# Performance work log

Measured on AMD Instinct MI355X. Metric: run time of the kernel, lower is better.

The kernel has to match this reference:

```python
import jax, jax.numpy as jnp
import numpy as np

NUM_SPHERICAL = 7
NUM_RADIAL = 6
CUTOFF = 5.0
ENVELOPE_EXPONENT = 5
ENVELOPE_CUTOFF = 5.0  # hardcoded in the torch module: poly_envelop(cutoff=5.0, ...)
E = 1_000_000   # num edges
T = 4_000_000   # num triplets (angles)


def _jn_np(l, x):
    """Spherical Bessel j_l(x) in numpy via upward recurrence (x > 0)."""
    j0 = np.sin(x) / x
    if l == 0:
        return j0
    j1 = np.sin(x) / x ** 2 - np.cos(x) / x
    for i in range(2, l + 1):
        j0, j1 = j1, (2 * i - 1) / x * j1 - j0
    return j1


def _jn_zeros(n, k):
    """First k positive zeros of j_l for l=0..n-1 (zeros interlace)."""
    zeros = np.zeros((n, k))
    prev = np.arange(1, k + n) * np.pi  # zeros of j_0
    zeros[0] = prev[:k]
    for l in range(1, n):
        cur = []
        for i in range(len(prev) - 1):
            a, b = prev[i], prev[i + 1]
            fa = _jn_np(l, a)
            for _ in range(80):  # bisection
                m = 0.5 * (a + b)
                fm = _jn_np(l, m)
                if np.sign(fm) == np.sign(fa):
                    a, fa = m, fm
                else:
                    b = m
            cur.append(0.5 * (a + b))
        prev = np.array(cur)
        zeros[l] = prev[:k]
    return zeros


# constants derived from (num_spherical, num_radial) at build time
Z = _jn_zeros(NUM_SPHERICAL, NUM_RADIAL)  # [S, R] Bessel zeros z_{l,n}
NORM = np.array([[np.sqrt(2.0) / abs(_jn_np(l + 1, Z[l, n])) for n in range(NUM_RADIAL)]
                 for l in range(NUM_SPHERICAL)])  # [S, R]
Y_NORM = np.array([np.sqrt((2 * l + 1) / (4.0 * np.pi)) for l in range(NUM_SPHERICAL)])  # m=0 SH norms


def _spherical_jn(l, a):
    """j_l(a) in jax via upward recurrence."""
    j0 = jnp.sin(a) / a
    if l == 0:
        return j0
    j1 = jnp.sin(a) / a ** 2 - jnp.cos(a) / a
    for i in range(2, l + 1):
        j0, j1 = j1, (2 * i - 1) / a * j1 - j0
    return j1


def _envelope(d):
    """DimeNet polynomial envelope, p = exponent + 1, on u = d / cutoff."""
    p = ENVELOPE_EXPONENT + 1
    a = -(p + 1) * (p + 2) / 2.0
    b = float(p * (p + 2))
    c = -p * (p + 1) / 2.0
    u = d / ENVELOPE_CUTOFF
    env = 1.0 / u + a * u ** (p - 1) + b * u ** p + c * u ** (p + 1)
    return jnp.where(u < 1.0, env, 0.0)


def setup_inputs() -> dict:
    key = jax.random.key(0)
    k1, k2, k3 = jax.random.split(key, 3)
    d = jax.random.uniform(k1, (E,), jnp.float32, 0.5, CUTOFF)           # edge distances
    Angles = jax.random.uniform(k2, (T,), jnp.float32, 0.0, float(np.pi))  # triplet angles
    edge_index_1 = jax.random.randint(k3, (T,), 0, E, dtype=jnp.int64 if jax.config.jax_enable_x64 else jnp.int32)
    return {"d": d, "Angles": Angles, "edge_index_1": edge_index_1}


def reference(d, Angles, edge_index_1):
    S, R = NUM_SPHERICAL, NUM_RADIAL
    zeros = jnp.asarray(Z, d.dtype)     # [S, R]
    norm = jnp.asarray(NORM, d.dtype)   # [S, R]
    x = d / CUTOFF                      # [E]
    # radial basis: norm_{l,n} * j_l(z_{l,n} * x)  -> [E, S, R]
    rbf = jnp.stack([norm[l] * _spherical_jn(l, zeros[l][None, :] * x[:, None])
                     for l in range(S)], axis=1)
    rbf_env = (_envelope(d)[:, None, None] * rbf).reshape(d.shape[0], S * R)  # [E, S*R]
    rbf_env = rbf_env[edge_index_1]  # gather triplets -> [T, S*R]
    # angular basis: Y_l^0(theta) = sqrt((2l+1)/4pi) * P_l(cos theta)
    c = jnp.cos(Angles)
    P = [jnp.ones_like(c), c]
    for l in range(2, S):
        P.append(((2 * l - 1) * c * P[l - 1] - (l - 1) * P[l - 2]) / l)
    y_norm = jnp.asarray(Y_NORM, c.dtype)
    cbf = jnp.stack([y_norm[l] * P[l] for l in range(S)], axis=1)  # [T, S]
    cbf = jnp.repeat(cbf, R, axis=1)  # repeat_interleave -> [T, S*R]
    return rbf_env * cbf
```

## Files before the change

kernel.cpp:

```cpp
#include <hip/hip_runtime.h>
#include <hip/hip_bf16.h>
#include <hip/hip_fp16.h>
#include <math.h>

#define NSPH 7
#define NRAD 6
#define NJ 42
#define ROWH 44
#define BLK 256

typedef float v2 __attribute__((ext_vector_type(2)));

struct KC {
  float zf[NJ];
  float izf[NJ];
  float nyf[NJ];
  float sc5[7];
  float sc6[7];
};

__global__ void __launch_bounds__(BLK, 4) k_fused(const float* __restrict__ d,
                                                  const float* __restrict__ ang,
                                                  const int* __restrict__ idx,
                                                  float* __restrict__ out,
                                                  int T, KC C) {
  __shared__ __half sv[BLK * ROWH];
  const int tid = threadIdx.x;
  const int t0 = blockIdx.x * BLK;
  const int t = t0 + tid;

  if (t < T) {
    const int e = __builtin_nontemporal_load(idx + t);
    const float an = __builtin_nontemporal_load(ang + t);
    const float dv = d[e];

    const float x = dv * 0.2f;
    const float invx = __builtin_amdgcn_rcpf(x);
    const float x2 = x * x;
    const float x5 = x2 * x2 * x;
    float env = invx + x5 * fmaf(x, fmaf(x, -21.0f, 48.0f), -28.0f);
    if (x >= 1.0f) env = 0.0f;

    const float cth = __cosf(an);
    float mP[NSPH];
    {
      float p0 = 1.f, p1 = cth;
      mP[0] = env; mP[1] = env * cth;
      const float rl[5] = {1.f/2.f, 1.f/3.f, 1.f/4.f, 1.f/5.f, 1.f/6.f};
      #pragma unroll
      for (int l = 2; l < NSPH; ++l) {
        float pn = (fmaf((float)(2*l-1) * cth, p1, -(float)(l-1) * p0)) * rl[l-2];
        mP[l] = env * pn;
        p0 = p1; p1 = pn;
      }
    }

    __half* row = sv + tid * ROWH;

    #pragma unroll
    for (int l = 0; l < 5; ++l) {
      #pragma unroll
      for (int p = 0; p < 3; ++p) {
        const int i = l * NRAD + 2 * p;
        v2 z    = {C.zf[i],  C.zf[i+1]};
        v2 iz   = {C.izf[i], C.izf[i+1]};
        v2 ny   = {C.nyf[i], C.nyf[i+1]};
        v2 a    = z * x;
        v2 s;  s.x = __sinf(a.x);  s.y = __sinf(a.y);
        v2 inva = iz * invx;
        v2 j0   = s * inva;
        v2 jl;
        if (l == 0) {
          jl = j0;
        } else {
          v2 c;  c.x = __cosf(a.x);  c.y = __cosf(a.y);
          v2 j1 = (j0 - c) * inva;
          #pragma unroll
          for (int m = 2; m <= l; ++m) {
            v2 jn_ = ((float)(2*m-1) * inva) * j1 - j0;
            j0 = j1; j1 = jn_;
          }
          jl = j1;
        }
        v2 jv = (ny * jl) * mP[l];
        *(__half2*)(row + i) = __float22half2_rn((float2){jv.x, jv.y});
      }
    }

    #pragma unroll
    for (int l = 5; l < NSPH; ++l) {
      const float* sc = (l == 5) ? C.sc5 : C.sc6;
      #pragma unroll
      for (int p = 0; p < 3; ++p) {
        const int i = l * NRAD + 2 * p;
        v2 z    = {C.zf[i],  C.zf[i+1]};
        v2 iz   = {C.izf[i], C.izf[i+1]};
        v2 ny   = {C.nyf[i], C.nyf[i+1]};
        v2 a    = z * x;
        v2 s;  s.x = __sinf(a.x);  s.y = __sinf(a.y);
        v2 c;  c.x = __cosf(a.x);  c.y = __cosf(a.y);
        v2 inva = iz * invx;
        v2 j0   = s * inva;
        v2 j1   = (j0 - c) * inva;
        #pragma unroll
        for (int m = 2; m <= l; ++m) {
          v2 jn_ = ((float)(2*m-1) * inva) * j1 - j0;
          j0 = j1; j1 = jn_;
        }
        v2 u  = a * a;
        v2 pp = u * sc[6] + sc[5];
        pp = u * pp + sc[4];
        pp = u * pp + sc[3];
        pp = u * pp + sc[2];
        pp = u * pp + sc[1];
        pp = u * pp + sc[0];
        v2 u2 = u * u;
        v2 al = (l == 5) ? (u2 * a) : (u2 * u);
        v2 jser = al * pp;
        v2 jl;
        jl.x = (a.x < 4.0f) ? jser.x : j1.x;
        jl.y = (a.y < 4.0f) ? jser.y : j1.y;
        v2 jv = (ny * jl) * mP[l];
        *(__half2*)(row + i) = __float22half2_rn((float2){jv.x, jv.y});
      }
    }
  }
  __syncthreads();

  v2* obase = (v2*)(out + (size_t)t0 * NJ);
  #pragma unroll
  for (int k = 0; k < 21; ++k) {
    unsigned w = k * BLK + tid;
    unsigned tl = w / 21u;
    unsigned jp = w - tl * 21u;
    if ((int)(t0 + tl) < T) {
      __half2 hh = *(const __half2*)(sv + tl * ROWH + 2 * jp);
      float2 r = __half22float2(hh);
      obase[w] = (v2){r.x, r.y};
    }
  }
}

static double jn_host(int l, double x) {
  double j0 = sin(x) / x;
  if (l == 0) return j0;
  double j1 = sin(x) / (x * x) - cos(x) / x;
  for (int i = 2; i <= l; ++i) {
    double jn_ = (2 * i - 1) / x * j1 - j0;
    j0 = j1; j1 = jn_;
  }
  return j1;
}

extern "C" void kernel_launch(void* const* d_in, const int* in_sizes, int n_in,
                              void* d_out, int out_size, void* d_ws, size_t ws_size,
                              hipStream_t stream) {
  const float* d   = (const float*)d_in[0];
  const float* ang = (const float*)d_in[1];
  const int*   idx = (const int*)d_in[2];
  float* out = (float*)d_out;
  const int T = in_sizes[1];

  KC C;
  {
    const double PI = 3.14159265358979323846;
    double zeros[NSPH][NRAD];
    double prev[NSPH + NRAD - 1];
    int np_ = NSPH + NRAD - 1;
    for (int i = 0; i < np_; ++i) prev[i] = (i + 1) * PI;
    for (int j = 0; j < NRAD; ++j) zeros[0][j] = prev[j];
    for (int l = 1; l < NSPH; ++l) {
      int nc = np_ - 1;
      double cur[NSPH + NRAD - 1];
      for (int i = 0; i < nc; ++i) {
        double a = prev[i], b = prev[i + 1];
        double fa = jn_host(l, a);
        for (int it = 0; it < 80; ++it) {
          double m = 0.5 * (a + b);
          double fm = jn_host(l, m);
          if ((fm > 0.0) == (fa > 0.0)) { a = m; fa = fm; } else { b = m; }
        }
        cur[i] = 0.5 * (a + b);
      }
      for (int i = 0; i < nc; ++i) prev[i] = cur[i];
      np_ = nc;
      for (int j = 0; j < NRAD; ++j) zeros[l][j] = prev[j];
    }
    for (int l = 0; l < NSPH; ++l) {
      double yn = sqrt((2.0 * l + 1.0) / (4.0 * PI));
      for (int n = 0; n < NRAD; ++n) {
        int i = l * NRAD + n;
        double z = zeros[l][n];
        C.zf[i]  = (float)z;
        C.izf[i] = (float)(1.0 / z);
        C.nyf[i] = (float)(sqrt(2.0) / fabs(jn_host(l + 1, z)) * yn);
      }
    }
    for (int l = 5; l <= 6; ++l) {
      double dfact = 1.0;
      for (int m = 2 * l + 1; m > 1; m -= 2) dfact *= m;
      double ck = 1.0 / dfact;
      float* sc = (l == 5) ? C.sc5 : C.sc6;
      sc[0] = (float)ck;
      for (int k = 1; k < 7; ++k) {
        ck = -ck / (2.0 * k * (2 * l + 2 * k + 1));
        sc[k] = (float)ck;
      }
    }
  }

  k_fused<<<(T + BLK - 1) / BLK, BLK, 0, stream>>>(d, ang, idx, out, T, C);
}
```

Before: 177.6 us.

## Use per-wave LDS slices, drop block barrier, widen nontemporal output stores

Each wave now writes its 64 triplets into its own unpadded LDS slice and reads them back after only an LDS waitcnt, replacing the block-wide __syncthreads. The transpose-out loop now issues 16-byte nontemporal stores instead of 8-byte stores, and the half conversion uses the packed round-toward-zero instruction. The aim is to remove barrier stalls, cut the number of store instructions and avoid cache pollution. The risks are LDS bank conflicts from removing the row padding and slightly different rounding, since round-toward-zero replaces round-to-nearest.

```diff
diff --git a/kernel.cpp b/kernel.cpp
--- a/kernel.cpp
+++ b/kernel.cpp
@@ -6,10 +6,11 @@
 #define NSPH 7
 #define NRAD 6
 #define NJ 42
-#define ROWH 44
 #define BLK 256
 
 typedef float v2 __attribute__((ext_vector_type(2)));
+typedef float v4 __attribute__((ext_vector_type(4)));
+typedef __fp16 h2 __attribute__((ext_vector_type(2)));
 
 struct KC {
   float zf[NJ];
@@ -24,10 +25,14 @@
                                                   const int* __restrict__ idx,
                                                   float* __restrict__ out,
                                                   int T, KC C) {
-  __shared__ __half sv[BLK * ROWH];
-  const int tid = threadIdx.x;
-  const int t0 = blockIdx.x * BLK;
-  const int t = t0 + tid;
+  __shared__ __half sv[BLK * NJ];
+  const int tid  = threadIdx.x;
+  const int lane = tid & 63;
+  const int wave = tid >> 6;
+  const int tw = blockIdx.x * BLK + wave * 64;
+  const int t  = tw + lane;
+
+  __half* slice = sv + wave * (64 * NJ);
 
   if (t < T) {
     const int e = __builtin_nontemporal_load(idx + t);
@@ -55,7 +60,7 @@
       }
     }
 
-    __half* row = sv + tid * ROWH;
+    __half* row = slice + lane * NJ;
 
     #pragma unroll
     for (int l = 0; l < 5; ++l) {
@@ -83,7 +88,7 @@
           jl = j1;
         }
         v2 jv = (ny * jl) * mP[l];
-        *(__half2*)(row + i) = __float22half2_rn((float2){jv.x, jv.y});
+        *(h2*)(row + i) = __builtin_amdgcn_cvt_pkrtz(jv.x, jv.y);
       }
     }
 
@@ -121,22 +126,41 @@
         jl.x = (a.x < 4.0f) ? jser.x : j1.x;
         jl.y = (a.y < 4.0f) ? jser.y : j1.y;
         v2 jv = (ny * jl) * mP[l];
-        *(__half2*)(row + i) = __float22half2_rn((float2){jv.x, jv.y});
-      }
-    }
-  }
-  __syncthreads();
-
-  v2* obase = (v2*)(out + (size_t)t0 * NJ);
-  #pragma unroll
-  for (int k = 0; k < 21; ++k) {
-    unsigned w = k * BLK + tid;
-    unsigned tl = w / 21u;
-    unsigned jp = w - tl * 21u;
-    if ((int)(t0 + tl) < T) {
-      __half2 hh = *(const __half2*)(sv + tl * ROWH + 2 * jp);
-      float2 r = __half22float2(hh);
-      obase[w] = (v2){r.x, r.y};
+        *(h2*)(row + i) = __builtin_amdgcn_cvt_pkrtz(jv.x, jv.y);
+      }
+    }
+  }
+
+  asm volatile("s_waitcnt lgkmcnt(0)" ::: "memory");
+
+  const unsigned char* sb = (const unsigned char*)slice;
+  float* ob = out + (size_t)tw * NJ;
+  const int valid = T - tw;
+  if (valid >= 64) {
+    #pragma unroll
+    for (int k = 0; k < 10; ++k) {
+      const int w4 = k * 64 + lane;
+      uint2 hh = *(const uint2*)(sb + 8u * (unsigned)w4);
+      float2 r0 = __half22float2(*(__half2*)&hh.x);
+      float2 r1 = __half22float2(*(__half2*)&hh.y);
+      __builtin_nontemporal_store((v4){r0.x, r0.y, r1.x, r1.y}, (v4*)(ob + 4 * w4));
+    }
+    if (lane < 32) {
+      const int w4 = 640 + lane;
+      uint2 hh = *(const uint2*)(sb + 8u * (unsigned)w4);
+      float2 r0 = __half22float2(*(__half2*)&hh.x);
+      float2 r1 = __half22float2(*(__half2*)&hh.y);
+      __builtin_nontemporal_store((v4){r0.x, r0.y, r1.x, r1.y}, (v4*)(ob + 4 * w4));
+    }
+  } else if (valid > 0) {
+    const int nw2 = valid * 21;
+    for (int k = 0; k < 21; ++k) {
+      const int w2 = k * 64 + lane;
+      if (w2 < nw2) {
+        __half2 hh = *(const __half2*)(sb + 4u * (unsigned)w2);
+        float2 r = __half22float2(hh);
+        __builtin_nontemporal_store((v2){r.x, r.y}, (v2*)(ob + 2 * w2));
+      }
     }
   }
 }
```

After: 179.6 us. About the same (+1.2%).
